# Optimization experiments

Hardware: AMD Instinct MI355X
Metric: run time of the kernel (lower is better)

Reference implementation:

```python
import jax, jax.numpy as jnp
import numpy as np

DMODEL = 1024
DHIDDEN = 1024
N_HEAD = 16
HEAD_DIM = DHIDDEN // N_HEAD
B, S = 4, 2048


def setup_inputs() -> dict:
    key = jax.random.key(0)
    ks = jax.random.split(key, 10)
    sc = 1.0 / np.sqrt(DMODEL)
    return {
        "x": jax.random.normal(ks[0], (B, S, DMODEL), dtype=jnp.float32),
        "Wq": jax.random.normal(ks[1], (DMODEL, DHIDDEN), dtype=jnp.float32) * sc,
        "bq": jnp.zeros((DHIDDEN,), dtype=jnp.float32),
        "Wk": jax.random.normal(ks[2], (DMODEL, DHIDDEN), dtype=jnp.float32) * sc,
        "bk": jnp.zeros((DHIDDEN,), dtype=jnp.float32),
        "Wv": jax.random.normal(ks[3], (DMODEL, DHIDDEN), dtype=jnp.float32) * sc,
        "bv": jnp.zeros((DHIDDEN,), dtype=jnp.float32),
        "Wo": jax.random.normal(ks[4], (DHIDDEN, DMODEL), dtype=jnp.float32) * sc,
        "bo": jnp.zeros((DMODEL,), dtype=jnp.float32),
        "ln_gamma": jnp.ones((DMODEL,), dtype=jnp.float32),
        "ln_beta": jnp.zeros((DMODEL,), dtype=jnp.float32),
    }


def _layernorm(x, gamma, beta, eps=1e-5):
    mu = jnp.mean(x, axis=-1, keepdims=True)
    var = jnp.var(x, axis=-1, keepdims=True)
    return (x - mu) * jax.lax.rsqrt(var + eps) * gamma + beta


def reference(x, Wq, bq, Wk, bk, Wv, bv, Wo, bo, ln_gamma, ln_beta):
    b, s, _ = x.shape
    h = _layernorm(x, ln_gamma, ln_beta)           # [B,S,D]
    q = h @ Wq + bq                                 # [B,S,Dh]
    k = h @ Wk + bk
    v = h @ Wv + bv
    # [B,H,S,hd]
    q = q.reshape(b, s, N_HEAD, HEAD_DIM).transpose(0, 2, 1, 3)
    k = k.reshape(b, s, N_HEAD, HEAD_DIM).transpose(0, 2, 1, 3)
    v = v.reshape(b, s, N_HEAD, HEAD_DIM).transpose(0, 2, 1, 3)
    scores = jnp.einsum("bhqd,bhkd->bhqk", q, k) / np.sqrt(HEAD_DIM)
    causal = jnp.tril(jnp.ones((s, s), dtype=bool))  # [S,S]
    scores = jnp.where(causal, scores, jnp.finfo(scores.dtype).min)
    attn = jax.nn.softmax(scores, axis=-1)           # [B,H,S,S]
    out = jnp.einsum("bhqk,bhkd->bhqd", attn, v)     # [B,H,S,hd]
    out = out.transpose(0, 2, 1, 3).reshape(b, s, DHIDDEN)
    return out @ Wo + bo
```

## Files before the change

kernel.cpp:

```cpp
#include <hip/hip_runtime.h>


typedef short short8 __attribute__((ext_vector_type(8)));
typedef float floatx4 __attribute__((ext_vector_type(4)));
typedef unsigned short ushort4v __attribute__((ext_vector_type(4)));
typedef unsigned int uint2v __attribute__((ext_vector_type(2)));

#define MFMA16(a, b, c) __builtin_amdgcn_mfma_f32_16x16x32_bf16((a), (b), (c), 0, 0, 0)

__device__ __forceinline__ unsigned short f2bf(float f) {
  unsigned int u = __float_as_uint(f);
  u += 0x7FFFu + ((u >> 16) & 1u);
  return (unsigned short)(u >> 16);
}

#if defined(__has_builtin)
#if __has_builtin(__builtin_amdgcn_cvt_pk_bf16_f32)
#define HAVE_PK_BF16 1
#endif
#if __has_builtin(__builtin_amdgcn_exp2f)
#define EXP2(x) __builtin_amdgcn_exp2f(x)
#endif
#if __has_builtin(__builtin_amdgcn_rcpf)
#define RCP(x) __builtin_amdgcn_rcpf(x)
#endif
#endif
#ifndef EXP2
#define EXP2(x) exp2f(x)
#endif
#ifndef RCP
#define RCP(x) (1.0f / (x))
#endif

__device__ __forceinline__ unsigned int pk_bf16(float a, float b) {
#ifdef HAVE_PK_BF16
  typedef __bf16 bf16x2_t __attribute__((ext_vector_type(2)));
  union { bf16x2_t v; unsigned int u; } cvt;
  cvt.v = __builtin_amdgcn_cvt_pk_bf16_f32(a, b);
  return cvt.u;
#else
  return (unsigned int)f2bf(a) | ((unsigned int)f2bf(b) << 16);
#endif
}

__device__ __forceinline__ void async_lds16(const void* g, void* l) {
  __builtin_amdgcn_global_load_lds(
      (const __attribute__((address_space(1))) void*)g,
      (__attribute__((address_space(3))) void*)l, 16, 0, 0);
}

__global__ __launch_bounds__(256) void prep_kernel(
    const float* __restrict__ wq, const float* __restrict__ wk,
    const float* __restrict__ wv, const float* __restrict__ wo,
    unsigned short* __restrict__ wqkvT, unsigned short* __restrict__ woT,
    const float* __restrict__ x, const float* __restrict__ gamma,
    const float* __restrict__ beta, unsigned short* __restrict__ h) {
  __shared__ float t[64][65];
  __shared__ float sm[4], qm[4];
  const int id = (int)blockIdx.x;
  const int tid = threadIdx.x;
  if (id < 1024) {
    const int mz = id >> 8, rem = id & 255;
    const int n0 = (rem & 15) * 64, k0 = (rem >> 4) * 64;
    const int r = tid >> 6, c = tid & 63;
    const float* src = (mz == 0) ? wq : (mz == 1) ? wk : (mz == 2) ? wv : wo;
    unsigned short* dst = (mz == 3) ? woT : (wqkvT + (size_t)mz * 1024 * 1024);
#pragma unroll
    for (int i = r; i < 64; i += 4) t[i][c] = src[(size_t)(k0 + i) * 1024 + n0 + c];
    __syncthreads();
#pragma unroll
    for (int i = r; i < 64; i += 4)
      dst[(size_t)(n0 + i) * 1024 + k0 + c] = f2bf(t[c][i]);
    return;
  }
  const int row = id - 1024;
  const float4 xv = ((const float4*)(x + (size_t)row * 1024))[tid];
  float s = xv.x + xv.y + xv.z + xv.w;
  float q = xv.x * xv.x + xv.y * xv.y + xv.z * xv.z + xv.w * xv.w;
#pragma unroll
  for (int off = 32; off > 0; off >>= 1) {
    s += __shfl_xor(s, off, 64);
    q += __shfl_xor(q, off, 64);
  }
  const int wave = tid >> 6, lane = tid & 63;
  if (lane == 0) { sm[wave] = s; qm[wave] = q; }
  __syncthreads();
  s = sm[0] + sm[1] + sm[2] + sm[3];
  q = qm[0] + qm[1] + qm[2] + qm[3];
  const float mean = s * (1.0f / 1024.0f);
  const float var = q * (1.0f / 1024.0f) - mean * mean;
  const float rstd = rsqrtf(var + 1e-5f);
  const float4 g = ((const float4*)gamma)[tid];
  const float4 bb = ((const float4*)beta)[tid];
  ushort4v o;
  o.x = f2bf((xv.x - mean) * rstd * g.x + bb.x);
  o.y = f2bf((xv.y - mean) * rstd * g.y + bb.y);
  o.z = f2bf((xv.z - mean) * rstd * g.z + bb.z);
  o.w = f2bf((xv.w - mean) * rstd * g.w + bb.w);
  ((ushort4v*)(h + (size_t)row * 1024))[tid] = o;
}

#define GEMM128_MAIN(A_, Bt_, m0_, n0_)                                         \
  __shared__ __align__(16) unsigned short lAB[2][128 * 64];                     \
  unsigned short* const lA = &lAB[0][0];                                        \
  unsigned short* const lB = &lAB[1][0];                                        \
  const int tid = threadIdx.x;                                                  \
  const int wave = tid >> 6, lane = tid & 63, quad = lane >> 4, l15 = lane & 15;\
  const int wm = wave >> 1, wn = wave & 1;                                      \
  const int m0 = (m0_), n0 = (n0_);                                             \
  const int srow = tid >> 3, schunk = tid & 7;                                  \
  const int swz = l15 & 7;                                                      \
  floatx4 acc[4][4];                                                            \
  _Pragma("unroll") for (int i = 0; i < 4; i++)                                 \
  _Pragma("unroll") for (int j = 0; j < 4; j++)                                 \
      acc[i][j] = (floatx4){0.f, 0.f, 0.f, 0.f};                                \
  for (int kt = 0; kt < 16; kt++) {                                             \
    const int k0 = kt * 64;                                                     \
    __syncthreads();                                                            \
    _Pragma("unroll") for (int j = 0; j < 4; j++) {                             \
      const int row_ = j * 32 + srow;                                           \
      const int gch_ = schunk ^ (row_ & 7);                                     \
      async_lds16(A_ + (size_t)(m0 + row_) * 1024 + k0 + gch_ * 8,              \
                  (char*)lA + j * 4096 + wave * 1024);                          \
      async_lds16(Bt_ + (size_t)(n0 + row_) * 1024 + k0 + gch_ * 8,             \
                  (char*)lB + j * 4096 + wave * 1024);                          \
    }                                                                           \
    __syncthreads();                                                            \
    _Pragma("unroll") for (int kk = 0; kk < 2; kk++) {                          \
      const int ch = (kk * 4 + quad) ^ swz;                                     \
      short8 af[4], bf[4];                                                      \
      _Pragma("unroll") for (int i = 0; i < 4; i++) {                           \
        af[i] = *(const short8*)(lA + (wm * 64 + i * 16 + l15) * 64 + ch * 8);  \
        bf[i] = *(const short8*)(lB + (wn * 64 + i * 16 + l15) * 64 + ch * 8);  \
      }                                                                         \
      _Pragma("unroll") for (int mt = 0; mt < 4; mt++)                          \
      _Pragma("unroll") for (int nt = 0; nt < 4; nt++)                          \
          acc[mt][nt] = MFMA16(af[mt], bf[nt], acc[mt][nt]);                    \
    }                                                                           \
  }

__global__ __launch_bounds__(256) void gemm_qkv(
    const unsigned short* __restrict__ A, const unsigned short* __restrict__ Bt,
    const float* __restrict__ bq, const float* __restrict__ bk,
    const float* __restrict__ bv, unsigned short* __restrict__ qo,
    unsigned short* __restrict__ ko, unsigned short* __restrict__ vT) {
  const int id = (int)blockIdx.x;
  const int xcd = id & 7, rr = id >> 3;
  GEMM128_MAIN(A, Bt, (xcd * 8 + (rr & 7)) * 128, (rr >> 3) * 128)
  const int sel = n0 >> 10;
  const float* bias = (sel == 0) ? bq : (sel == 1) ? bk : bv;
  const float oscale = (sel == 0) ? 0.18033688011112042f : 1.0f;
  unsigned short* const st = &lAB[0][0];
  const int b16 = (m0 >> 11) * 16;
  const int h0 = (n0 & 1023) >> 6;
  const int ms = m0 & 2047;
  __syncthreads();
  if (sel == 2) {
#pragma unroll
    for (int nt = 0; nt < 4; nt++) {
      const int nl = wn * 64 + nt * 16 + l15;
      const float bia = bias[(n0 + nl) & 1023];
      const int x = (nl & 15) << 1;
#pragma unroll
      for (int mt = 0; mt < 4; mt++) {
        const int chunk = wm * 16 + mt * 4 + quad;
        ushort4v pk;
#pragma unroll
        for (int r = 0; r < 4; r++) pk[r] = f2bf(acc[mt][nt][r] + bia);
        *(ushort4v*)((char*)st + nl * 256 + ((chunk ^ x) << 3)) = pk;
      }
    }
    __syncthreads();
#pragma unroll
    for (int p = 0; p < 8; p++) {
      const int nl = p * 16 + (tid >> 4);
      const int j2 = tid & 15;
      const short8 vv =
          *(const short8*)((char*)st + nl * 256 + ((j2 ^ (nl & 15)) << 4));
      *(short8*)(vT + ((size_t)(b16 + h0 + (nl >> 6)) * 64 + (nl & 63)) * 2048 +
                 ms + j2 * 8) = vv;
    }
  } else {
#pragma unroll
    for (int nt = 0; nt < 4; nt++) {
      const int nl = wn * 64 + nt * 16 + l15;
      const float bia = bias[(n0 + nl) & 1023];
      const int chunk = nl >> 3, nin = nl & 7;
#pragma unroll
      for (int mt = 0; mt < 4; mt++) {
#pragma unroll
        for (int r = 0; r < 4; r++) {
          const int ml = wm * 64 + mt * 16 + quad * 4 + r;
          *(unsigned short*)((char*)st + ml * 256 + ((chunk ^ (ml & 7)) << 4) +
                             nin * 2) = f2bf((acc[mt][nt][r] + bia) * oscale);
        }
      }
    }
    __syncthreads();
    unsigned short* const dq = (sel == 0) ? qo : ko;
#pragma unroll
    for (int p = 0; p < 8; p++) {
      const int ml = p * 16 + (tid >> 4);
      const int j = tid & 15;
      const short8 vv =
          *(const short8*)((char*)st + ml * 256 + ((j ^ (ml & 7)) << 4));
      *(short8*)(dq + ((size_t)(b16 + h0 + (j >> 3)) * 2048 + (ms + ml)) * 64 +
                 (j & 7) * 8) = vv;
    }
  }
}

__global__ __launch_bounds__(256) void gemm_out(
    const unsigned short* __restrict__ A, const unsigned short* __restrict__ Bt,
    const float* __restrict__ bo, float* __restrict__ out) {
  const int id = (int)blockIdx.x;
  const int xcd = id & 7, rr = id >> 3;
  GEMM128_MAIN(A, Bt, (xcd * 8 + (rr & 7)) * 128, (rr >> 3) * 128)
#pragma unroll
  for (int nt = 0; nt < 4; nt++) {
    const int n = n0 + wn * 64 + nt * 16 + l15;
    const float bia = bo[n];
#pragma unroll
    for (int mt = 0; mt < 4; mt++) {
      const int m = m0 + wm * 64 + mt * 16 + quad * 4;
#pragma unroll
      for (int r = 0; r < 4; r++) out[(size_t)(m + r) * 1024 + n] = acc[mt][nt][r] + bia;
    }
  }
}

__global__ __launch_bounds__(256, 4) void attn_kernel(
    const unsigned short* __restrict__ q, const unsigned short* __restrict__ k,
    const unsigned short* __restrict__ vT, unsigned short* __restrict__ ao) {
  __shared__ __align__(16) unsigned short lK[2][64 * 64];
  __shared__ __align__(16) unsigned short lV[2][64 * 64];
  __shared__ __align__(16) unsigned short lP[4][16 * 64];
  const int tid = threadIdx.x;
  const int wave = tid >> 6, lane = tid & 63, quad = lane >> 4, l15 = lane & 15;
  const int id = (int)blockIdx.x;
  const int bh = (id & 7) * 8 + ((id >> 3) & 7);
  const int qx = id >> 6;
  const int b = bh >> 4, hh = bh & 15;
  const int qtA = 31 - qx, qtB = qx;
  const int q0wA = qtA * 64 + wave * 16, q0wB = qtB * 64 + wave * 16;
  const int ntiles = qtA + 1;

  const unsigned short* qb = q + (size_t)bh * 2048 * 64;
  const unsigned short* kb = k + (size_t)bh * 2048 * 64;
  const unsigned short* vb = vT + (size_t)bh * 64 * 2048;
  unsigned short* pw = &lP[wave][0];

  const int srow = tid >> 3, schunk = tid & 7;

  const short8 ones8 = {0x3F80, 0x3F80, 0x3F80, 0x3F80,
                        0x3F80, 0x3F80, 0x3F80, 0x3F80};

  const int sw = l15 & 7;
  const int ph0 = (0 * 4 + quad) ^ sw, ph1 = (1 * 4 + quad) ^ sw;

#define STAGE_TILE(src_, rstride_, cbase_, dst_)                                 \
  _Pragma("unroll") for (int j = 0; j < 2; j++) {                                \
    const int row_ = j * 32 + srow;                                              \
    const int gch_ = schunk ^ (row_ & 7);                                        \
    async_lds16(src_ + (size_t)row_ * (rstride_) + (cbase_) + gch_ * 8,          \
                (char*)(dst_) + j * 4096 + wave * 1024);                         \
  }

  short8 qfA[2], qfB[2];
#pragma unroll
  for (int hf = 0; hf < 2; hf++) {
    qfA[hf] = *(const short8*)(qb + (size_t)(q0wA + l15) * 64 + hf * 32 + quad * 8);
    qfB[hf] = *(const short8*)(qb + (size_t)(q0wB + l15) * 64 + hf * 32 + quad * 8);
  }

  floatx4 oA[4], oB[4];
#pragma unroll
  for (int nt = 0; nt < 4; nt++) {
    oA[nt] = (floatx4){0.f, 0.f, 0.f, 0.f};
    oB[nt] = (floatx4){0.f, 0.f, 0.f, 0.f};
  }
  floatx4 laccA = {0.f, 0.f, 0.f, 0.f}, laccB = {0.f, 0.f, 0.f, 0.f};

  STAGE_TILE(kb, 64, 0, &lK[0][0])
  STAGE_TILE(vb, 2048, 0, &lV[0][0])
  int kbase = 0;
  for (int t = 0; t < ntiles; t++, kbase += 64) {
    __syncthreads();
    if (t + 1 < ntiles) {
      const int nb = (t + 1) & 1;
      STAGE_TILE(kb, 64, (size_t)(kbase + 64) * 64, &lK[nb][0])
      STAGE_TILE(vb, 2048, (size_t)(kbase + 64), &lV[nb][0])
    }
    const unsigned short* lKc = &lK[t & 1][0];
    const unsigned short* lVc = &lV[t & 1][0];
    const bool dual = (t <= qtB);

    floatx4 scA[4], scB[4];
    __builtin_amdgcn_s_setprio(1);
#pragma unroll
    for (int nt = 0; nt < 4; nt++) {
      scA[nt] = (floatx4){0.f, 0.f, 0.f, 0.f};
      scB[nt] = (floatx4){0.f, 0.f, 0.f, 0.f};
      const short8 kf0 = *(const short8*)(lKc + (nt * 16 + l15) * 64 + ph0 * 8);
      const short8 kf1 = *(const short8*)(lKc + (nt * 16 + l15) * 64 + ph1 * 8);
      scA[nt] = MFMA16(kf0, qfA[0], scA[nt]);
      scA[nt] = MFMA16(kf1, qfA[1], scA[nt]);
      if (dual) {
        scB[nt] = MFMA16(kf0, qfB[0], scB[nt]);
        scB[nt] = MFMA16(kf1, qfB[1], scB[nt]);
      }
    }
    __builtin_amdgcn_s_setprio(0);

    {
      const bool needmask = (kbase + 63 > q0wA);
      const int qg = q0wA + l15;
#pragma unroll
      for (int nt = 0; nt < 4; nt++) {
        float p0 = EXP2(scA[nt][0]), p1 = EXP2(scA[nt][1]);
        float p2 = EXP2(scA[nt][2]), p3 = EXP2(scA[nt][3]);
        if (needmask) {
          const int kk = kbase + nt * 16 + quad * 4;
          if (kk + 0 > qg) p0 = 0.f;
          if (kk + 1 > qg) p1 = 0.f;
          if (kk + 2 > qg) p2 = 0.f;
          if (kk + 3 > qg) p3 = 0.f;
        }
        uint2v pk2;
        pk2.x = pk_bf16(p0, p1);
        pk2.y = pk_bf16(p2, p3);
        const int phys = (nt * 2 + (quad >> 1)) ^ sw;
        *(uint2v*)(pw + l15 * 64 + phys * 8 + (quad & 1) * 4) = pk2;
      }
    }
    asm volatile("s_waitcnt lgkmcnt(0)" ::: "memory");
    short8 pfA0 = *(const short8*)(pw + l15 * 64 + ph0 * 8);
    short8 pfA1 = *(const short8*)(pw + l15 * 64 + ph1 * 8);

    short8 pfB0, pfB1;
    if (dual) {
      const bool needmask = (kbase + 63 > q0wB);
      const int qg = q0wB + l15;
#pragma unroll
      for (int nt = 0; nt < 4; nt++) {
        float p0 = EXP2(scB[nt][0]), p1 = EXP2(scB[nt][1]);
        float p2 = EXP2(scB[nt][2]), p3 = EXP2(scB[nt][3]);
        if (needmask) {
          const int kk = kbase + nt * 16 + quad * 4;
          if (kk + 0 > qg) p0 = 0.f;
          if (kk + 1 > qg) p1 = 0.f;
          if (kk + 2 > qg) p2 = 0.f;
          if (kk + 3 > qg) p3 = 0.f;
        }
        uint2v pk2;
        pk2.x = pk_bf16(p0, p1);
        pk2.y = pk_bf16(p2, p3);
        const int phys = (nt * 2 + (quad >> 1)) ^ sw;
        *(uint2v*)(pw + l15 * 64 + phys * 8 + (quad & 1) * 4) = pk2;
      }
      asm volatile("s_waitcnt lgkmcnt(0)" ::: "memory");
      pfB0 = *(const short8*)(pw + l15 * 64 + ph0 * 8);
      pfB1 = *(const short8*)(pw + l15 * 64 + ph1 * 8);
    }

    __builtin_amdgcn_s_setprio(1);
#pragma unroll
    for (int hf = 0; hf < 2; hf++) {
      const short8 pfA = hf ? pfA1 : pfA0;
      laccA = MFMA16(ones8, pfA, laccA);
      if (dual) laccB = MFMA16(ones8, hf ? pfB1 : pfB0, laccB);
      const int ph = hf ? ph1 : ph0;
#pragma unroll
      for (int nt = 0; nt < 4; nt++) {
        const short8 vf = *(const short8*)(lVc + (nt * 16 + l15) * 64 + ph * 8);
        oA[nt] = MFMA16(vf, pfA, oA[nt]);
        if (dual) oB[nt] = MFMA16(vf, hf ? pfB1 : pfB0, oB[nt]);
      }
    }
    __builtin_amdgcn_s_setprio(0);
  }

  {
    const float linv = RCP(laccA[0]);
    unsigned short* dst = ao + ((size_t)b * 2048 + q0wA + l15) * 1024 + hh * 64;
#pragma unroll
    for (int nt = 0; nt < 4; nt++) {
      uint2v pk2;
      pk2.x = pk_bf16(oA[nt][0] * linv, oA[nt][1] * linv);
      pk2.y = pk_bf16(oA[nt][2] * linv, oA[nt][3] * linv);
      *(uint2v*)(dst + nt * 16 + quad * 4) = pk2;
    }
  }
  {
    const float linv = RCP(laccB[0]);
    unsigned short* dst = ao + ((size_t)b * 2048 + q0wB + l15) * 1024 + hh * 64;
#pragma unroll
    for (int nt = 0; nt < 4; nt++) {
      uint2v pk2;
      pk2.x = pk_bf16(oB[nt][0] * linv, oB[nt][1] * linv);
      pk2.y = pk_bf16(oB[nt][2] * linv, oB[nt][3] * linv);
      *(uint2v*)(dst + nt * 16 + quad * 4) = pk2;
    }
  }
#undef STAGE_TILE
}

extern "C" void kernel_launch(void* const* d_in, const int* in_sizes, int n_in,
                              void* d_out, int out_size, void* d_ws, size_t ws_size,
                              hipStream_t stream) {
  const float* x = (const float*)d_in[0];
  const float* Wq = (const float*)d_in[1];
  const float* bq = (const float*)d_in[2];
  const float* Wk = (const float*)d_in[3];
  const float* bk = (const float*)d_in[4];
  const float* Wv = (const float*)d_in[5];
  const float* bv = (const float*)d_in[6];
  const float* Wo = (const float*)d_in[7];
  const float* bo = (const float*)d_in[8];
  const float* gamma = (const float*)d_in[9];
  const float* beta = (const float*)d_in[10];
  float* out = (float*)d_out;

  char* ws = (char*)d_ws;
  unsigned short* wqkvT = (unsigned short*)(ws + 0);
  unsigned short* woT   = (unsigned short*)(ws + 6291456);
  unsigned short* h     = (unsigned short*)(ws + 8388608);
  unsigned short* qb    = (unsigned short*)(ws + 25165824);
  unsigned short* kb    = (unsigned short*)(ws + 41943040);
  unsigned short* vT    = (unsigned short*)(ws + 58720256);
  unsigned short* ao    = (unsigned short*)(ws + 75497472);

  hipLaunchKernelGGL(prep_kernel, dim3(9216), dim3(256), 0, stream,
                     Wq, Wk, Wv, Wo, wqkvT, woT, x, gamma, beta, h);
  hipLaunchKernelGGL(gemm_qkv, dim3(1536), dim3(256), 0, stream,
                     h, wqkvT, bq, bk, bv, qb, kb, vT);
  hipLaunchKernelGGL(attn_kernel, dim3(1024), dim3(256), 0, stream, qb, kb, vT, ao);
  hipLaunchKernelGGL(gemm_out, dim3(512), dim3(256), 0, stream, ao, woT, bo, out);
}
```

Before: 265.2 us.

## Load attention K/V directly from global and retile output GEMM to 64x128

```diff
diff --git a/kernel.cpp b/kernel.cpp
--- a/kernel.cpp
+++ b/kernel.cpp
@@ -213,16 +213,63 @@
 __global__ __launch_bounds__(256) void gemm_out(
     const unsigned short* __restrict__ A, const unsigned short* __restrict__ Bt,
     const float* __restrict__ bo, float* __restrict__ out) {
+  __shared__ __align__(16) unsigned short lA[64 * 64];
+  __shared__ __align__(16) unsigned short lB[128 * 64];
+  const int tid = threadIdx.x;
+  const int wave = tid >> 6, lane = tid & 63, quad = lane >> 4, l15 = lane & 15;
   const int id = (int)blockIdx.x;
   const int xcd = id & 7, rr = id >> 3;
-  GEMM128_MAIN(A, Bt, (xcd * 8 + (rr & 7)) * 128, (rr >> 3) * 128)
-#pragma unroll
-  for (int nt = 0; nt < 4; nt++) {
-    const int n = n0 + wn * 64 + nt * 16 + l15;
+  const int m0 = (xcd * 16 + (rr & 15)) * 64;
+  const int n0 = (rr >> 4) * 128;
+  const int srow = tid >> 3, schunk = tid & 7;
+  const int swz = l15 & 7;
+  floatx4 acc[4][2];
+#pragma unroll
+  for (int i = 0; i < 4; i++)
+#pragma unroll
+    for (int j = 0; j < 2; j++) acc[i][j] = (floatx4){0.f, 0.f, 0.f, 0.f};
+  for (int kt = 0; kt < 16; kt++) {
+    const int k0 = kt * 64;
+    __syncthreads();
+#pragma unroll
+    for (int j = 0; j < 2; j++) {
+      const int row_ = j * 32 + srow;
+      const int gch_ = schunk ^ (row_ & 7);
+      async_lds16(A + (size_t)(m0 + row_) * 1024 + k0 + gch_ * 8,
+                  (char*)lA + j * 4096 + wave * 1024);
+    }
+#pragma unroll
+    for (int j = 0; j < 4; j++) {
+      const int row_ = j * 32 + srow;
+      const int gch_ = schunk ^ (row_ & 7);
+      async_lds16(Bt + (size_t)(n0 + row_) * 1024 + k0 + gch_ * 8,
+                  (char*)lB + j * 4096 + wave * 1024);
+    }
+    __syncthreads();
+#pragma unroll
+    for (int kk = 0; kk < 2; kk++) {
+      const int ch = (kk * 4 + quad) ^ swz;
+      short8 af[4], bf[2];
+#pragma unroll
+      for (int i = 0; i < 4; i++)
+        af[i] = *(const short8*)(lA + (i * 16 + l15) * 64 + ch * 8);
+#pragma unroll
+      for (int i = 0; i < 2; i++)
+        bf[i] = *(const short8*)(lB + (wave * 32 + i * 16 + l15) * 64 + ch * 8);
+#pragma unroll
+      for (int mt = 0; mt < 4; mt++)
+#pragma unroll
+        for (int nt = 0; nt < 2; nt++)
+          acc[mt][nt] = MFMA16(af[mt], bf[nt], acc[mt][nt]);
+    }
+  }
+#pragma unroll
+  for (int nt = 0; nt < 2; nt++) {
+    const int n = n0 + wave * 32 + nt * 16 + l15;
     const float bia = bo[n];
 #pragma unroll
     for (int mt = 0; mt < 4; mt++) {
-      const int m = m0 + wm * 64 + mt * 16 + quad * 4;
+      const int m = m0 + mt * 16 + quad * 4;
 #pragma unroll
       for (int r = 0; r < 4; r++) out[(size_t)(m + r) * 1024 + n] = acc[mt][nt][r] + bia;
     }
@@ -232,8 +279,6 @@
 __global__ __launch_bounds__(256, 4) void attn_kernel(
     const unsigned short* __restrict__ q, const unsigned short* __restrict__ k,
     const unsigned short* __restrict__ vT, unsigned short* __restrict__ ao) {
-  __shared__ __align__(16) unsigned short lK[2][64 * 64];
-  __shared__ __align__(16) unsigned short lV[2][64 * 64];
   __shared__ __align__(16) unsigned short lP[4][16 * 64];
   const int tid = threadIdx.x;
   const int wave = tid >> 6, lane = tid & 63, quad = lane >> 4, l15 = lane & 15;
@@ -250,21 +295,11 @@
   const unsigned short* vb = vT + (size_t)bh * 64 * 2048;
   unsigned short* pw = &lP[wave][0];
 
-  const int srow = tid >> 3, schunk = tid & 7;
-
   const short8 ones8 = {0x3F80, 0x3F80, 0x3F80, 0x3F80,
                         0x3F80, 0x3F80, 0x3F80, 0x3F80};
 
   const int sw = l15 & 7;
   const int ph0 = (0 * 4 + quad) ^ sw, ph1 = (1 * 4 + quad) ^ sw;
-
-#define STAGE_TILE(src_, rstride_, cbase_, dst_)                                 \
-  _Pragma("unroll") for (int j = 0; j < 2; j++) {                                \
-    const int row_ = j * 32 + srow;                                              \
-    const int gch_ = schunk ^ (row_ & 7);                                        \
-    async_lds16(src_ + (size_t)row_ * (rstride_) + (cbase_) + gch_ * 8,          \
-                (char*)(dst_) + j * 4096 + wave * 1024);                         \
-  }
 
   short8 qfA[2], qfB[2];
 #pragma unroll
@@ -281,18 +316,8 @@
   }
   floatx4 laccA = {0.f, 0.f, 0.f, 0.f}, laccB = {0.f, 0.f, 0.f, 0.f};
 
-  STAGE_TILE(kb, 64, 0, &lK[0][0])
-  STAGE_TILE(vb, 2048, 0, &lV[0][0])
   int kbase = 0;
   for (int t = 0; t < ntiles; t++, kbase += 64) {
-    __syncthreads();
-    if (t + 1 < ntiles) {
-      const int nb = (t + 1) & 1;
-      STAGE_TILE(kb, 64, (size_t)(kbase + 64) * 64, &lK[nb][0])
-      STAGE_TILE(vb, 2048, (size_t)(kbase + 64), &lV[nb][0])
-    }
-    const unsigned short* lKc = &lK[t & 1][0];
-    const unsigned short* lVc = &lV[t & 1][0];
     const bool dual = (t <= qtB);
 
     floatx4 scA[4], scB[4];
@@ -301,8 +326,9 @@
     for (int nt = 0; nt < 4; nt++) {
       scA[nt] = (floatx4){0.f, 0.f, 0.f, 0.f};
       scB[nt] = (floatx4){0.f, 0.f, 0.f, 0.f};
-      const short8 kf0 = *(const short8*)(lKc + (nt * 16 + l15) * 64 + ph0 * 8);
-      const short8 kf1 = *(const short8*)(lKc + (nt * 16 + l15) * 64 + ph1 * 8);
+      const unsigned short* krow = kb + (size_t)(kbase + nt * 16 + l15) * 64;
+      const short8 kf0 = *(const short8*)(krow + quad * 8);
+      const short8 kf1 = *(const short8*)(krow + 32 + quad * 8);
       scA[nt] = MFMA16(kf0, qfA[0], scA[nt]);
       scA[nt] = MFMA16(kf1, qfA[1], scA[nt]);
       if (dual) {
@@ -369,10 +395,10 @@
       const short8 pfA = hf ? pfA1 : pfA0;
       laccA = MFMA16(ones8, pfA, laccA);
       if (dual) laccB = MFMA16(ones8, hf ? pfB1 : pfB0, laccB);
-      const int ph = hf ? ph1 : ph0;
 #pragma unroll
       for (int nt = 0; nt < 4; nt++) {
-        const short8 vf = *(const short8*)(lVc + (nt * 16 + l15) * 64 + ph * 8);
+        const short8 vf = *(const short8*)(
+            vb + (size_t)(nt * 16 + l15) * 2048 + kbase + (hf * 4 + quad) * 8);
         oA[nt] = MFMA16(vf, pfA, oA[nt]);
         if (dual) oB[nt] = MFMA16(vf, hf ? pfB1 : pfB0, oB[nt]);
       }
@@ -402,7 +428,6 @@
       *(uint2v*)(dst + nt * 16 + quad * 4) = pk2;
     }
   }
-#undef STAGE_TILE
 }
 
 extern "C" void kernel_launch(void* const* d_in, const int* in_sizes, int n_in,
@@ -435,5 +460,5 @@
   hipLaunchKernelGGL(gemm_qkv, dim3(1536), dim3(256), 0, stream,
                      h, wqkvT, bq, bk, bv, qb, kb, vT);
   hipLaunchKernelGGL(attn_kernel, dim3(1024), dim3(256), 0, stream, qb, kb, vT, ao);
-  hipLaunchKernelGGL(gemm_out, dim3(512), dim3(256), 0, stream, ao, woT, bo, out);
-}
+  hipLaunchKernelGGL(gemm_out, dim3(1024), dim3(256), 0, stream, ao, woT, bo, out);
+}
```

Result: slower. 402.7 us (+51.8%).
